# Performance work log

Hardware: AMD Instinct MI355X
Metric: run time of the kernel (lower is better)

## Reference

```python
import jax, jax.numpy as jnp
import numpy as np
import math

B, S, D = 4, 2048, 2048
NH, NKV, HD = 16, 4, 128

def setup_inputs() -> dict:
    key = jax.random.key(0)
    ks = jax.random.split(key, 9)
    s = 1.0 / math.sqrt(D)
    return {
        "x": jax.random.normal(ks[0], (B, S, D), dtype=jnp.float32),
        "Wq": jax.random.normal(ks[1], (D, NH * HD), dtype=jnp.float32) * s,
        "bq": jnp.zeros((NH * HD,), dtype=jnp.float32),
        "Wk": jax.random.normal(ks[2], (D, NKV * HD), dtype=jnp.float32) * s,
        "bk": jnp.zeros((NKV * HD,), dtype=jnp.float32),
        "Wv": jax.random.normal(ks[3], (D, NKV * HD), dtype=jnp.float32) * s,
        "bv": jnp.zeros((NKV * HD,), dtype=jnp.float32),
        "Wo": jax.random.normal(ks[4], (D, D), dtype=jnp.float32) * s,
        "bo": jnp.zeros((D,), dtype=jnp.float32),
    }

def reference(x, Wq, bq, Wk, bk, Wv, bv, Wo, bo):
    b, s, _ = x.shape
    group = NH // NKV
    q = (x @ Wq + bq).reshape(b, s, NH, HD).transpose(0, 2, 1, 3)   # [B,NH,S,HD]
    k = (x @ Wk + bk).reshape(b, s, NKV, HD).transpose(0, 2, 1, 3)  # [B,NKV,S,HD]
    v = (x @ Wv + bv).reshape(b, s, NKV, HD).transpose(0, 2, 1, 3)
    # repeat_interleave KV heads to match query heads
    k = jnp.repeat(k, group, axis=1)  # [B,NH,S,HD]
    v = jnp.repeat(v, group, axis=1)
    scores = jnp.einsum("bhqd,bhkd->bhqk", q, k) / math.sqrt(HD)
    causal = jnp.tril(jnp.ones((s, s), dtype=bool))
    scores = jnp.where(causal, scores, -jnp.inf)
    probs = jax.nn.softmax(scores, axis=-1)  # dropout p=0.0 -> identity
    out = jnp.einsum("bhqk,bhkd->bhqd", probs, v)
    out = out.transpose(0, 2, 1, 3).reshape(b, s, NH * HD)
    return out @ Wo + bo
```

## Files before the change

kernel.cpp:

```cpp
#include <hip/hip_runtime.h>
#include <hip/hip_bf16.h>

typedef __attribute__((ext_vector_type(4)))  float f32x4;
typedef __attribute__((ext_vector_type(16))) float f32x16;
typedef __attribute__((ext_vector_type(8)))  short s16x8;
typedef __attribute__((ext_vector_type(4)))  short s16x4;
typedef __attribute__((ext_vector_type(4)))  float fvec4;

__device__ __forceinline__ short f2bf(float f) {
    union { float f; unsigned u; } x; x.f = f;
    unsigned r = x.u + 0x7fffu + ((x.u >> 16) & 1u);
    return (short)(r >> 16);
}

__device__ __forceinline__ short cvtbf(float f) {
    __hip_bfloat16 t = __float2bfloat16(f);
    return *reinterpret_cast<short*>(&t);
}

__device__ __forceinline__ void gload_lds16(const short* g, short* lds) {
    __builtin_amdgcn_global_load_lds(
        (const __attribute__((address_space(1))) void*)g,
        (__attribute__((address_space(3))) void*)lds, 16, 0, 0);
}

__global__ __launch_bounds__(256) void prep(const float* __restrict__ x,
                                            const float* __restrict__ Wq,
                                            const float* __restrict__ Wk,
                                            const float* __restrict__ Wv,
                                            short* __restrict__ Xb,
                                            short* __restrict__ WqT,
                                            short* __restrict__ WkvT) {
    const int bid = blockIdx.x, tid = threadIdx.x;
    if (bid < 8192) {
        size_t i = ((size_t)bid * 256 + tid) * 8;
        fvec4 a = *(const fvec4*)&x[i];
        fvec4 b = *(const fvec4*)&x[i + 4];
        s16x8 o;
        o[0] = f2bf(a[0]); o[1] = f2bf(a[1]); o[2] = f2bf(a[2]); o[3] = f2bf(a[3]);
        o[4] = f2bf(b[0]); o[5] = f2bf(b[1]); o[6] = f2bf(b[2]); o[7] = f2bf(b[3]);
        *(s16x8*)&Xb[i] = o;
        return;
    }
    const float* W; short* Wt; int N, local;
    if (bid < 12288)      { W = Wq; Wt = WqT;                      N = 2048; local = bid - 8192; }
    else if (bid < 13312) { W = Wk; Wt = WkvT;                     N = 512;  local = bid - 12288; }
    else                  { W = Wv; Wt = WkvT + (size_t)512 * 2048; N = 512; local = bid - 13312; }
    __shared__ float tile[32][33];
    const int k0 = (local & 63) * 32, n0 = (local >> 6) * 32;
    const int tx = tid & 31, ty = tid >> 5;
    #pragma unroll
    for (int i = 0; i < 4; ++i) {
        int k = ty + i * 8;
        tile[k][tx] = W[(size_t)(k0 + k) * N + n0 + tx];
    }
    __syncthreads();
    #pragma unroll
    for (int i = 0; i < 4; ++i) {
        int n = ty + i * 8;
        Wt[(size_t)(n0 + n) * 2048 + k0 + tx] = f2bf(tile[tx][n]);
    }
}

__global__ __launch_bounds__(256) void tconv(const float* __restrict__ W,
                                             short* __restrict__ Wt,
                                             int K, int N) {
    __shared__ float tile[32][33];
    const int k0 = blockIdx.x * 32, n0 = blockIdx.y * 32;
    const int tx = threadIdx.x & 31, ty = threadIdx.x >> 5;
    #pragma unroll
    for (int i = 0; i < 4; ++i) {
        int k = ty + i * 8;
        tile[k][tx] = W[(size_t)(k0 + k) * N + n0 + tx];
    }
    __syncthreads();
    #pragma unroll
    for (int i = 0; i < 4; ++i) {
        int n = ty + i * 8;
        Wt[(size_t)(n0 + n) * K + k0 + tx] = f2bf(tile[tx][n]);
    }
}

template<int MODE>
__global__ __launch_bounds__(512, 1) void gemm256(const short* __restrict__ A,
                                                  const short* __restrict__ Bt,
                                                  const float* __restrict__ bias,
                                                  void* __restrict__ Cv,
                                                  int M, int N, int K) {
    __shared__ __align__(16) short As[2][16384];
    __shared__ __align__(16) short Bs[2][16384];
    const int tid = threadIdx.x, lane = tid & 63, w = tid >> 6;
    const int wr = w >> 2, wc = w & 3;
    const int lr = lane & 15, g = lane >> 4;
    const int bid = blockIdx.x;
    const int xcd = bid & 7, ii = bid >> 3;
    const int m0 = (xcd * 4 + (ii & 3)) * 256;
    const int n0 = (ii >> 2) * 256;
    const int r0 = w * 8 + (lane >> 3);
    const int sw = ((lane & 7) ^ ((lane >> 3) & 7)) * 8;
    const int swr = lr & 7;

    const short* ga = A  + (size_t)(m0 + r0) * K + sw;
    const short* gb = Bt + (size_t)(n0 + r0) * K + sw;

    f32x4 acc[8][4] = {};
    const int NT = K >> 6;

#define STAGE256(d, t) do {                                                     \
    const int kk0_ = (t) << 6;                                                  \
    _Pragma("unroll")                                                           \
    for (int it_ = 0; it_ < 4; ++it_) {                                         \
        gload_lds16(ga + (size_t)(it_ * 64) * K + kk0_, &As[d][it_ * 4096 + w * 512]); \
        gload_lds16(gb + (size_t)(it_ * 64) * K + kk0_, &Bs[d][it_ * 4096 + w * 512]); \
    }                                                                           \
} while (0)

    STAGE256(0, 0);

    for (int T = 0; T < NT; ++T) {
        const int d = T & 1;
        if (T + 1 < NT) {
            STAGE256((T + 1) & 1, T + 1);
            asm volatile("s_waitcnt vmcnt(8)" ::: "memory");
        } else {
            asm volatile("s_waitcnt vmcnt(0)" ::: "memory");
        }
        __builtin_amdgcn_s_barrier();
        __builtin_amdgcn_sched_barrier(0);
        s16x8 bf[4][2];
        #pragma unroll
        for (int n = 0; n < 4; ++n)
            #pragma unroll
            for (int kk = 0; kk < 2; ++kk)
                bf[n][kk] = *(const s16x8*)&Bs[d][(wc * 64 + n * 16 + lr) * 64 +
                                                 (((kk << 2) | g) ^ swr) * 8];
        #pragma unroll
        for (int p = 0; p < 4; ++p) {
            s16x8 af[2][2];
            #pragma unroll
            for (int mm = 0; mm < 2; ++mm)
                #pragma unroll
                for (int kk = 0; kk < 2; ++kk)
                    af[mm][kk] = *(const s16x8*)&As[d][(wr * 128 + (p * 2 + mm) * 16 + lr) * 64 +
                                                      (((kk << 2) | g) ^ swr) * 8];
            __builtin_amdgcn_s_setprio(1);
            #pragma unroll
            for (int kk = 0; kk < 2; ++kk)
                #pragma unroll
                for (int mm = 0; mm < 2; ++mm)
                    #pragma unroll
                    for (int n = 0; n < 4; ++n)
                        acc[p * 2 + mm][n] = __builtin_amdgcn_mfma_f32_16x16x32_bf16(
                            af[mm][kk], bf[n][kk], acc[p * 2 + mm][n], 0, 0, 0);
            __builtin_amdgcn_s_setprio(0);
            __builtin_amdgcn_s_barrier();
        }
        __builtin_amdgcn_sched_barrier(0);
    }
    #pragma unroll
    for (int m = 0; m < 8; ++m)
        #pragma unroll
        for (int j = 0; j < 4; ++j) {
            int row = m0 + wr * 128 + m * 16 + g * 4 + j;
            #pragma unroll
            for (int n = 0; n < 4; ++n) {
                int col = n0 + wc * 64 + n * 16 + lr;
                float v = acc[m][n][j] + bias[col];
                if constexpr (MODE == 1) ((short*)Cv)[(size_t)row * N + col] = f2bf(v);
                else                     ((float*)Cv)[(size_t)row * N + col] = v;
            }
        }
#undef STAGE256
}

__global__ __launch_bounds__(512, 1) void gemm256kv(const short* __restrict__ A,
                                                    const short* __restrict__ Bt,
                                                    const float* __restrict__ bias_k,
                                                    const float* __restrict__ bias_v,
                                                    short* __restrict__ Kout,
                                                    short* __restrict__ Vout,
                                                    int K) {
    __shared__ __align__(16) short As[2][16384];
    __shared__ __align__(16) short Bs[2][8192];
    const int tid = threadIdx.x, lane = tid & 63, w = tid >> 6;
    const int wr = w >> 1, wc = w & 1;
    const int lr = lane & 15, g = lane >> 4;
    const int bid = blockIdx.x;
    const int xcd = bid & 7, ii = bid >> 3;
    const int m0 = (xcd * 4 + (ii & 3)) * 256;
    const int n0 = (ii >> 2) * 128;
    const int r0 = w * 8 + (lane >> 3);
    const int sw = ((lane & 7) ^ ((lane >> 3) & 7)) * 8;
    const int swr = lr & 7;

    const short* ga = A  + (size_t)(m0 + r0) * K + sw;
    const short* gb = Bt + (size_t)(n0 + r0) * K + sw;

    f32x4 acc[4][4] = {};
    const int NT = K >> 6;

#define STAGEKV(d, t) do {                                                      \
    const int kk0_ = (t) << 6;                                                  \
    _Pragma("unroll")                                                           \
    for (int it_ = 0; it_ < 4; ++it_)                                           \
        gload_lds16(ga + (size_t)(it_ * 64) * K + kk0_, &As[d][it_ * 4096 + w * 512]); \
    _Pragma("unroll")                                                           \
    for (int it_ = 0; it_ < 2; ++it_)                                           \
        gload_lds16(gb + (size_t)(it_ * 64) * K + kk0_, &Bs[d][it_ * 4096 + w * 512]); \
} while (0)

    STAGEKV(0, 0);

    for (int T = 0; T < NT; ++T) {
        const int d = T & 1;
        if (T + 1 < NT) {
            STAGEKV((T + 1) & 1, T + 1);
            asm volatile("s_waitcnt vmcnt(6)" ::: "memory");
        } else {
            asm volatile("s_waitcnt vmcnt(0)" ::: "memory");
        }
        __builtin_amdgcn_s_barrier();
        __builtin_amdgcn_sched_barrier(0);
        s16x8 bf[4][2];
        #pragma unroll
        for (int n = 0; n < 4; ++n)
            #pragma unroll
            for (int kk = 0; kk < 2; ++kk)
                bf[n][kk] = *(const s16x8*)&Bs[d][(wc * 64 + n * 16 + lr) * 64 +
                                                 (((kk << 2) | g) ^ swr) * 8];
        #pragma unroll
        for (int p = 0; p < 2; ++p) {
            s16x8 af[2][2];
            #pragma unroll
            for (int mm = 0; mm < 2; ++mm)
                #pragma unroll
                for (int kk = 0; kk < 2; ++kk)
                    af[mm][kk] = *(const s16x8*)&As[d][(wr * 64 + (p * 2 + mm) * 16 + lr) * 64 +
                                                      (((kk << 2) | g) ^ swr) * 8];
            __builtin_amdgcn_s_setprio(1);
            #pragma unroll
            for (int kk = 0; kk < 2; ++kk)
                #pragma unroll
                for (int mm = 0; mm < 2; ++mm)
                    #pragma unroll
                    for (int n = 0; n < 4; ++n)
                        acc[p * 2 + mm][n] = __builtin_amdgcn_mfma_f32_16x16x32_bf16(
                            af[mm][kk], bf[n][kk], acc[p * 2 + mm][n], 0, 0, 0);
            __builtin_amdgcn_s_setprio(0);
            __builtin_amdgcn_s_barrier();
        }
        __builtin_amdgcn_sched_barrier(0);
    }
    if (n0 < 512) {
        #pragma unroll
        for (int m = 0; m < 4; ++m)
            #pragma unroll
            for (int j = 0; j < 4; ++j) {
                int row = m0 + wr * 64 + m * 16 + g * 4 + j;
                #pragma unroll
                for (int n = 0; n < 4; ++n) {
                    int col = n0 + wc * 64 + n * 16 + lr;
                    Kout[(size_t)row * 512 + col] = f2bf(acc[m][n][j] + bias_k[col]);
                }
            }
    } else {
        #pragma unroll
        for (int m = 0; m < 4; ++m)
            #pragma unroll
            for (int n = 0; n < 4; ++n) {
                int vcol = n0 - 512 + wc * 64 + n * 16 + lr;
                int kvh = vcol >> 7, dd = vcol & 127;
                int row0 = m0 + wr * 64 + m * 16 + g * 4;
                int b = row0 >> 11, s0 = row0 & 2047;
                int s0p = (s0 & ~15) | (((s0 >> 2) & 1) << 3) | (((s0 >> 3) & 1) << 2);
                s16x4 o;
                #pragma unroll
                for (int j = 0; j < 4; ++j) o[j] = f2bf(acc[m][n][j] + bias_v[vcol]);
                *(s16x4*)&Vout[(((size_t)b * 4 + kvh) * 128 + dd) * 2048 + s0p] = o;
            }
    }
#undef STAGEKV
}

#define SC2 0.12751743f
#define MOFF (-48.0f * SC2)

__global__ __launch_bounds__(512, 1) void attn_kernel(const short* __restrict__ Q,
                                                      const short* __restrict__ Kg,
                                                      const short* __restrict__ Vtg,
                                                      short* __restrict__ Oa) {
    __shared__ __align__(16) short Klds[2][8192];
    __shared__ __align__(16) short Vlds[2][8192];
    const int tid = threadIdx.x;
    const int lane = tid & 63, w = tid >> 6;
    const int l31 = lane & 31, hi = lane >> 5, e7 = lane & 7;
    const int ve = hi ^ e7;

    const int bid = blockIdx.x;
    const int grp = bid & 15, j = bid >> 4;
    const int b = grp >> 2, kvh = grp & 3;
    const int h = kvh * 4 + (j & 3);
    const int qtp = (j >> 2) & 3, ph = j >> 4;
    const int qt = ph ? (3 - qtp) : (4 + qtp);
    const int qb = qt << 8;

    const int q_min = qb + w * 32;
    const int qg = q_min + l31;
    const size_t qrow = (size_t)b * 2048 + qg;

    s16x8 qf[8];
    #pragma unroll
    for (int c = 0; c < 8; ++c)
        qf[c] = *(const s16x8*)&Q[qrow * 2048 + h * 128 + c * 16 + hi * 8];

    f32x16 oacc[4] = {};
    float l_half = 0.f;

    const int nt = (qb >> 6) + 4;

    const short* Kbase = Kg + ((size_t)b * 2048) * 512 + kvh * 128;
    const short* Vbase = Vtg + ((size_t)(b * 4 + kvh)) * 128 * 2048;

    const int krow0 = w * 4 + (lane >> 4), kslot = lane & 15;
    const int vrow0 = w * 8 + (lane >> 3), vslot = lane & 7;

#define STAGE(buf, t) do {                                                        \
    const int kv0_ = (t) << 6;                                                    \
    _Pragma("unroll")                                                             \
    for (int s_ = 0; s_ < 2; ++s_) {                                              \
        int kr = s_ * 32 + krow0;                                                 \
        gload_lds16(Kbase + (size_t)(kv0_ + kr) * 512 + (kslot ^ (kr & 7)) * 8,   \
                    &Klds[buf][s_ * 4096 + w * 512]);                             \
        int vr = s_ * 64 + vrow0;                                                 \
        gload_lds16(Vbase + (size_t)vr * 2048 + kv0_ + (vslot ^ (vr & 7)) * 8,    \
                    &Vlds[buf][s_ * 4096 + w * 512]);                             \
    }                                                                             \
} while (0)

#define SMPV(sv, st, domask) do {                                                 \
    if (domask) {                                                                 \
        _Pragma("unroll")                                                         \
        for (int r = 0; r < 16; ++r) {                                            \
            const int rw = (r & 3) + 8 * (r >> 2) + 4 * hi;                       \
            if (rw > l31) sv[r] = -1e30f;                                         \
        }                                                                         \
    }                                                                             \
    _Pragma("unroll")                                                             \
    for (int r = 0; r < 16; ++r)                                                  \
        sv[r] = __builtin_amdgcn_exp2f(fmaf(sv[r], SC2, MOFF));                   \
    l_half += (((sv[0] + sv[1]) + (sv[2] + sv[3])) +                              \
               ((sv[4] + sv[5]) + (sv[6] + sv[7]))) +                             \
              (((sv[8] + sv[9]) + (sv[10] + sv[11])) +                            \
               ((sv[12] + sv[13]) + (sv[14] + sv[15])));                          \
    s16x8 pa0, pa1;                                                               \
    _Pragma("unroll")                                                             \
    for (int jj = 0; jj < 8; ++jj) { pa0[jj] = cvtbf(sv[jj]); pa1[jj] = cvtbf(sv[8 + jj]); } \
    const short* vb = &Vlds[cur][l31 * 64];                                       \
    _Pragma("unroll")                                                             \
    for (int dn = 0; dn < 4; ++dn) {                                              \
        s16x8 vf = *(const s16x8*)&vb[dn * 2048 + ((((st) << 2) ^ ve)) * 8];      \
        oacc[dn] = __builtin_amdgcn_mfma_f32_32x32x16_bf16(vf, pa0, oacc[dn], 0, 0, 0); \
    }                                                                             \
    _Pragma("unroll")                                                             \
    for (int dn = 0; dn < 4; ++dn) {                                              \
        s16x8 vf = *(const s16x8*)&vb[dn * 2048 + (((((st) << 2) | 2) ^ ve)) * 8];\
        oacc[dn] = __builtin_amdgcn_mfma_f32_32x32x16_bf16(vf, pa1, oacc[dn], 0, 0, 0); \
    }                                                                             \
} while (0)

    STAGE(0, 0);
    __syncthreads();

    int cur = 0;
    for (int t = 0; t < nt; ++t) {
        if (t + 1 < nt) STAGE(cur ^ 1, t + 1);
        const int kv0 = t << 6;
        const bool w0 = kv0 <= q_min;
        const bool w1 = kv0 + 32 <= q_min;
        f32x16 s0 = {}, s1 = {};
        if (w0) {
            const short* kb = &Klds[cur][l31 * 128];
            #pragma unroll
            for (int c = 0; c < 8; ++c) {
                s16x8 kf = *(const s16x8*)&kb[(((c << 1) ^ ve)) * 8];
                s0 = __builtin_amdgcn_mfma_f32_32x32x16_bf16(kf, qf[c], s0, 0, 0, 0);
            }
        }
        if (w1) {
            const short* kb = &Klds[cur][(32 + l31) * 128];
            #pragma unroll
            for (int c = 0; c < 8; ++c) {
                s16x8 kf = *(const s16x8*)&kb[(((c << 1) ^ ve)) * 8];
                s1 = __builtin_amdgcn_mfma_f32_32x32x16_bf16(kf, qf[c], s1, 0, 0, 0);
            }
        }
        if (w0) SMPV(s0, 0, (kv0 == q_min));
        if (w1) SMPV(s1, 1, (kv0 + 32 == q_min));
        __syncthreads();
        cur ^= 1;
    }
    const float l_run = l_half + __shfl_xor(l_half, 32);
    const float inv = 1.0f / l_run;
    const size_t obase = qrow * 2048 + h * 128;
    #pragma unroll
    for (int dn = 0; dn < 4; ++dn)
        #pragma unroll
        for (int u = 0; u < 4; ++u) {
            s16x4 o;
            #pragma unroll
            for (int jj = 0; jj < 4; ++jj) o[jj] = cvtbf(oacc[dn][u * 4 + jj] * inv);
            *(s16x4*)&Oa[obase + dn * 32 + u * 8 + hi * 4] = o;
        }
#undef STAGE
#undef SMPV
}

extern "C" void kernel_launch(void* const* d_in, const int* in_sizes, int n_in,
                              void* d_out, int out_size, void* d_ws, size_t ws_size,
                              hipStream_t stream) {
    const float* x  = (const float*)d_in[0];
    const float* Wq = (const float*)d_in[1];
    const float* bq = (const float*)d_in[2];
    const float* Wk = (const float*)d_in[3];
    const float* bk = (const float*)d_in[4];
    const float* Wv = (const float*)d_in[5];
    const float* bv = (const float*)d_in[6];
    const float* Wo = (const float*)d_in[7];
    const float* bo = (const float*)d_in[8];
    float* out = (float*)d_out;

    char* ws = (char*)d_ws;
    short* Xb  = (short*)(ws);
    short* Qb  = (short*)(ws + (size_t)33554432);
    short* Kb  = (short*)(ws + (size_t)67108864);
    short* Vt  = (short*)(ws + (size_t)75497472);
    short* WoT = (short*)(ws);
    char* dob = (char*)d_out;
    short* WqT  = (short*)(dob);
    short* WkvT = (short*)(dob + (size_t)8388608);

    const int M = 8192, D = 2048;

    prep<<<dim3(14336), 256, 0, stream>>>(x, Wq, Wk, Wv, Xb, WqT, WkvT);

    gemm256<1><<<dim3(256), 512, 0, stream>>>(Xb, WqT, bq, Qb, M, 2048, D);
    gemm256kv<<<dim3(256), 512, 0, stream>>>(Xb, WkvT, bk, bv, Kb, Vt, D);

    tconv<<<dim3(64, 64), 256, 0, stream>>>(Wo, WoT, D, D);

    attn_kernel<<<dim3(512), 512, 0, stream>>>(Qb, Kb, Vt, Qb);

    gemm256<0><<<dim3(256), 512, 0, stream>>>(Qb, WoT, bo, out, M, 2048, D);
}
```

Measured before the change: 321.4 us.

## Restructure gemm256 into 4-stage pipeline with K=32 slices

Replaces the double-buffered 64-wide K tile in the 256x256 GEMM with a four-slot ring of 32-wide K slices. Loads are issued three slices ahead, and there is one barrier per slice instead of several per tile, with a new XOR swizzle for the narrower rows. The goal is deeper prefetch to hide global-load latency and fewer intra-tile barriers. In exchange each slice has less MFMA work to cover the barrier and wait, and the A/B fragments are now all loaded before the MFMA block rather than interleaved with it.

```diff
diff --git a/kernel.cpp b/kernel.cpp
--- a/kernel.cpp
+++ b/kernel.cpp
@@ -87,8 +87,8 @@
                                                   const float* __restrict__ bias,
                                                   void* __restrict__ Cv,
                                                   int M, int N, int K) {
-    __shared__ __align__(16) short As[2][16384];
-    __shared__ __align__(16) short Bs[2][16384];
+    __shared__ __align__(16) short As[4][8192];
+    __shared__ __align__(16) short Bs[4][8192];
     const int tid = threadIdx.x, lane = tid & 63, w = tid >> 6;
     const int wr = w >> 2, wc = w & 3;
     const int lr = lane & 15, g = lane >> 4;
@@ -96,66 +96,50 @@
     const int xcd = bid & 7, ii = bid >> 3;
     const int m0 = (xcd * 4 + (ii & 3)) * 256;
     const int n0 = (ii >> 2) * 256;
-    const int r0 = w * 8 + (lane >> 3);
-    const int sw = ((lane & 7) ^ ((lane >> 3) & 7)) * 8;
-    const int swr = lr & 7;
-
-    const short* ga = A  + (size_t)(m0 + r0) * K + sw;
-    const short* gb = Bt + (size_t)(n0 + r0) * K + sw;
+    const int l2 = lane >> 2, l3 = lane & 3;
+    const int swz = (l3 ^ (l2 & 3)) * 8;
+    const int rsw = (g ^ (lr & 3)) * 8;
+
+    const short* gaw = A  + (size_t)(m0 + w * 32 + l2) * K + swz;
+    const short* gbw = Bt + (size_t)(n0 + w * 32 + l2) * K + swz;
 
     f32x4 acc[8][4] = {};
-    const int NT = K >> 6;
-
-#define STAGE256(d, t) do {                                                     \
-    const int kk0_ = (t) << 6;                                                  \
-    _Pragma("unroll")                                                           \
-    for (int it_ = 0; it_ < 4; ++it_) {                                         \
-        gload_lds16(ga + (size_t)(it_ * 64) * K + kk0_, &As[d][it_ * 4096 + w * 512]); \
-        gload_lds16(gb + (size_t)(it_ * 64) * K + kk0_, &Bs[d][it_ * 4096 + w * 512]); \
-    }                                                                           \
+    const int NH = K >> 5;
+
+#define ISSUE(h) do {                                                           \
+    const int s_ = (h) & 3;                                                     \
+    const int kh_ = (h) << 5;                                                   \
+    gload_lds16(gaw + kh_,                 &As[s_][(w * 2) * 512]);             \
+    gload_lds16(gaw + (size_t)16 * K + kh_, &As[s_][(w * 2 + 1) * 512]);        \
+    gload_lds16(gbw + kh_,                 &Bs[s_][(w * 2) * 512]);             \
+    gload_lds16(gbw + (size_t)16 * K + kh_, &Bs[s_][(w * 2 + 1) * 512]);        \
 } while (0)
 
-    STAGE256(0, 0);
-
-    for (int T = 0; T < NT; ++T) {
-        const int d = T & 1;
-        if (T + 1 < NT) {
-            STAGE256((T + 1) & 1, T + 1);
-            asm volatile("s_waitcnt vmcnt(8)" ::: "memory");
-        } else {
-            asm volatile("s_waitcnt vmcnt(0)" ::: "memory");
-        }
+    ISSUE(0); ISSUE(1); ISSUE(2);
+
+    for (int h = 0; h < NH; ++h) {
+        if (h + 2 < NH)      asm volatile("s_waitcnt vmcnt(8)" ::: "memory");
+        else if (h + 1 < NH) asm volatile("s_waitcnt vmcnt(4)" ::: "memory");
+        else                 asm volatile("s_waitcnt vmcnt(0)" ::: "memory");
         __builtin_amdgcn_s_barrier();
         __builtin_amdgcn_sched_barrier(0);
-        s16x8 bf[4][2];
+        if (h + 3 < NH) ISSUE(h + 3);
+        const int s = h & 3;
+        s16x8 bf[4], af[8];
         #pragma unroll
         for (int n = 0; n < 4; ++n)
-            #pragma unroll
-            for (int kk = 0; kk < 2; ++kk)
-                bf[n][kk] = *(const s16x8*)&Bs[d][(wc * 64 + n * 16 + lr) * 64 +
-                                                 (((kk << 2) | g) ^ swr) * 8];
-        #pragma unroll
-        for (int p = 0; p < 4; ++p) {
-            s16x8 af[2][2];
-            #pragma unroll
-            for (int mm = 0; mm < 2; ++mm)
-                #pragma unroll
-                for (int kk = 0; kk < 2; ++kk)
-                    af[mm][kk] = *(const s16x8*)&As[d][(wr * 128 + (p * 2 + mm) * 16 + lr) * 64 +
-                                                      (((kk << 2) | g) ^ swr) * 8];
-            __builtin_amdgcn_s_setprio(1);
-            #pragma unroll
-            for (int kk = 0; kk < 2; ++kk)
-                #pragma unroll
-                for (int mm = 0; mm < 2; ++mm)
-                    #pragma unroll
-                    for (int n = 0; n < 4; ++n)
-                        acc[p * 2 + mm][n] = __builtin_amdgcn_mfma_f32_16x16x32_bf16(
-                            af[mm][kk], bf[n][kk], acc[p * 2 + mm][n], 0, 0, 0);
-            __builtin_amdgcn_s_setprio(0);
-            __builtin_amdgcn_s_barrier();
-        }
-        __builtin_amdgcn_sched_barrier(0);
+            bf[n] = *(const s16x8*)&Bs[s][(wc * 64 + n * 16 + lr) * 32 + rsw];
+        #pragma unroll
+        for (int i = 0; i < 8; ++i)
+            af[i] = *(const s16x8*)&As[s][(wr * 128 + i * 16 + lr) * 32 + rsw];
+        __builtin_amdgcn_s_setprio(1);
+        #pragma unroll
+        for (int i = 0; i < 8; ++i)
+            #pragma unroll
+            for (int n = 0; n < 4; ++n)
+                acc[i][n] = __builtin_amdgcn_mfma_f32_16x16x32_bf16(
+                    af[i], bf[n], acc[i][n], 0, 0, 0);
+        __builtin_amdgcn_s_setprio(0);
     }
     #pragma unroll
     for (int m = 0; m < 8; ++m)
@@ -170,7 +154,7 @@
                 else                     ((float*)Cv)[(size_t)row * N + col] = v;
             }
         }
-#undef STAGE256
+#undef ISSUE
 }
 
 __global__ __launch_bounds__(512, 1) void gemm256kv(const short* __restrict__ A,
```

Result: slower. 330.6 us (+2.8%).
